# Kernel tuning notes

Measured on AMD Instinct MI355X. Metric: run time of the kernel, lower is better.

The kernel has to match this reference:

```python
import jax, jax.numpy as jnp
import numpy as np

N, E, F_IN, H, NC, NG = 50000, 800000, 256, 64, 4, 64

def setup_inputs() -> dict:
    key = jax.random.key(0)
    ks = jax.random.split(key, 12)
    inp = {
        'x': jax.random.normal(ks[0], (N, F_IN), dtype=jnp.float32),
        'edge_index': jax.random.randint(ks[1], (2, E), 0, N, dtype=jnp.int64),
        'batch': jnp.sort(jax.random.randint(ks[2], (N,), 0, NG, dtype=jnp.int64)),
        # GCNConv layer 1 and 2 (weight [in,out] + bias), Glorot-ish scale
        'W1': jax.random.normal(ks[3], (F_IN, H), dtype=jnp.float32) / np.sqrt(F_IN),
        'b1': jnp.zeros((H,), dtype=jnp.float32),
        'W2': jax.random.normal(ks[4], (H, H), dtype=jnp.float32) / np.sqrt(H),
        'b2': jnp.zeros((H,), dtype=jnp.float32),
        # MLP head
        'fc1_w': jax.random.normal(ks[5], (H, 128), dtype=jnp.float32) / np.sqrt(H),
        'fc1_b': jnp.zeros((128,), dtype=jnp.float32),
        'fc2_w': jax.random.normal(ks[6], (128, NC), dtype=jnp.float32) / np.sqrt(128),
        'fc2_b': jnp.zeros((NC,), dtype=jnp.float32),
    }
    return inp

def _gcn_conv(x, src, dst, W, b, n_nodes):
    # PyG GCNConv: add self-loops, symmetric norm D^-1/2 (A+I) D^-1/2, then X W + b
    h = x @ W  # [N, out]
    deg = jax.ops.segment_sum(jnp.ones_like(dst, dtype=h.dtype), dst, num_segments=n_nodes)
    dinv = jnp.where(deg > 0, jax.lax.rsqrt(deg), 0.0)
    norm = dinv[src] * dinv[dst]  # [E+N]
    msg = h[src] * norm[:, None]
    out = jax.ops.segment_sum(msg, dst, num_segments=n_nodes)
    return out + b

def reference(x, edge_index, batch, W1, b1, W2, b2, fc1_w, fc1_b, fc2_w, fc2_b):
    n = x.shape[0]
    loops = jnp.arange(n, dtype=edge_index.dtype)
    src = jnp.concatenate([edge_index[0], loops])
    dst = jnp.concatenate([edge_index[1], loops])
    h = jax.nn.relu(_gcn_conv(x, src, dst, W1, b1, n))
    h = jax.nn.relu(_gcn_conv(h, src, dst, W2, b2, n))
    # global_mean_pool over graph ids
    sums = jax.ops.segment_sum(h, batch, num_segments=NG)
    cnts = jax.ops.segment_sum(jnp.ones((n,), h.dtype), batch, num_segments=NG)
    pooled = sums / jnp.maximum(cnts, 1.0)[:, None]  # [NG, H]
    z = jax.nn.relu(pooled @ fc1_w + fc1_b)
    # dropout in eval mode = identity
    return z @ fc2_w + fc2_b  # [NG, NC]
```

## Files before the change

### kernel.cpp

```cpp
#include <hip/hip_runtime.h>


#define TPB 256
#define CHUNK_A 4096
#define BCAP 4608

typedef unsigned short bfu;

__device__ __forceinline__ float bf2f(bfu u) {
    union { unsigned u32; float f; } c; c.u32 = ((unsigned)u) << 16; return c.f;
}
__device__ __forceinline__ bfu f2bf(float f) {
    union { float f; unsigned u; } c; c.f = f;
    unsigned r = 0x7FFFu + ((c.u >> 16) & 1u);
    return (bfu)((c.u + r) >> 16);
}
__device__ __forceinline__ float blo(unsigned w) {
    union { unsigned u32; float f; } c; c.u32 = w << 16; return c.f;
}
__device__ __forceinline__ float bhi(unsigned w) {
    union { unsigned u32; float f; } c; c.u32 = w & 0xFFFF0000u; return c.f;
}


__global__ __launch_bounds__(TPB) void k_passA(const int* __restrict__ srcv,
                                               const int* __restrict__ dstv, int E,
                                               int* __restrict__ gcur,
                                               int* __restrict__ staged, int nbuck) {
    __shared__ int pk[CHUNK_A];
    __shared__ int hist[256];
    __shared__ int ebase[256];
    __shared__ int gbase[256];
    __shared__ int lcur[256];
    int t = threadIdx.x;
    int e0 = blockIdx.x * CHUNK_A;
    int e1 = e0 + CHUNK_A; if (e1 > E) e1 = E;

    hist[t] = 0; lcur[t] = 0;
    __syncthreads();
    for (int i = e0 + t; i < e1; i += TPB) atomicAdd(&hist[dstv[i] >> 8], 1);
    __syncthreads();
    int v = hist[t];
    ebase[t] = v;
    __syncthreads();
    for (int off = 1; off < 256; off <<= 1) {
        int u = (t >= off) ? ebase[t - off] : 0;
        __syncthreads();
        ebase[t] += u;
        __syncthreads();
    }
    ebase[t] -= v;
    if (t < nbuck && v > 0) gbase[t] = t * BCAP + atomicAdd(&gcur[t], v);
    __syncthreads();
    for (int i = e0 + t; i < e1; i += TPB) {
        int d = dstv[i];
        int s = srcv[i];
        int b = d >> 8;
        int r = atomicAdd(&lcur[b], 1);
        pk[ebase[b] + r] = (s << 8) | (d & 255);
    }
    __syncthreads();
    int wave = t >> 6, lane = t & 63;
    for (int b = wave; b < nbuck; b += 4) {
        int c = hist[b];
        int lb = ebase[b];
        int gb = gbase[b];
        for (int j = lane; j < c; j += 64) staged[gb + j] = pk[lb + j];
    }
}


__global__ __launch_bounds__(TPB) void k_passB(const int* __restrict__ staged,
                                               const int* __restrict__ gcur,
                                               int* __restrict__ csr_off,
                                               int* __restrict__ csr_src,
                                               float* __restrict__ dinv,
                                               int n, int nbuck) {
    __shared__ int pk[BCAP];
    __shared__ int soff[256];
    __shared__ int hist[256];
    __shared__ int nbase[256];
    __shared__ int cur[256];
    int b = blockIdx.x;
    int n0 = b << 8;
    int n1 = n0 + 256; if (n1 > n) n1 = n;
    int cnt = gcur[b];
    int t = threadIdx.x;

    int cv = (t < nbuck) ? gcur[t] : 0;
    soff[t] = cv;
    hist[t] = 0; cur[t] = 0;
    __syncthreads();
    for (int off = 1; off < 256; off <<= 1) {
        int u = (t >= off) ? soff[t - off] : 0;
        __syncthreads();
        soff[t] += u;
        __syncthreads();
    }
    int base = soff[b] - cnt;

    for (int i = t; i < cnt; i += TPB) pk[i] = staged[b * BCAP + i];
    __syncthreads();
    for (int i = t; i < cnt; i += TPB) atomicAdd(&hist[pk[i] & 255], 1);
    __syncthreads();
    int v = hist[t];
    nbase[t] = v;
    __syncthreads();
    for (int off = 1; off < 256; off <<= 1) {
        int u = (t >= off) ? nbase[t - off] : 0;
        __syncthreads();
        nbase[t] += u;
        __syncthreads();
    }
    nbase[t] -= v;
    if (n0 + t < n1) {
        csr_off[n0 + t] = base + nbase[t];
        dinv[n0 + t] = rsqrtf((float)(v + 1));
    }
    if (b == nbuck - 1 && t == 0) csr_off[n] = base + cnt;
    __syncthreads();
    for (int i = t; i < cnt; i += TPB) {
        int p = pk[i];
        int dloc = p & 255;
        int r = atomicAdd(&cur[dloc], 1);
        csr_src[base + nbase[dloc] + r] = p >> 8;
    }
}


template <int K, bool BF16A>
__global__ __launch_bounds__(TPB) void k_gemm(const void* __restrict__ Av,
                                              const float* __restrict__ W,
                                              const float* __restrict__ dinv,
                                              bfu* __restrict__ C, int n) {
    __shared__ __align__(16) float Wc[64 * 64];
    __shared__ __align__(16) float xr[64 * 68];
    const int t = threadIdx.x;
    const int wave = t >> 6, lane = t & 63;
    const int li = lane >> 4, lj = lane & 15;
    const int rl0 = wave * 16 + li * 4;
    const int rbase = blockIdx.x * 64;

    float acc[4][4] = {{0.f,0.f,0.f,0.f},{0.f,0.f,0.f,0.f},{0.f,0.f,0.f,0.f},{0.f,0.f,0.f,0.f}};

    for (int kc = 0; kc < K; kc += 64) {
        {
            const float4* wsv = (const float4*)(W + (size_t)kc * 64);
            float4* wd = (float4*)Wc;
#pragma unroll
            for (int q = 0; q < 4; q++) wd[t + q * 256] = wsv[t + q * 256];
        }
        {
            int rl = t >> 2;
            int kq = (t & 3) * 16;
            int r = rbase + rl;
            if (!BF16A) {
                const float* A = (const float*)Av;
#pragma unroll
                for (int m = 0; m < 16; m += 4) {
                    float4 xv;
                    if (r < n) xv = *(const float4*)&A[(size_t)r * K + kc + kq + m];
                    else       xv = make_float4(0.f, 0.f, 0.f, 0.f);
                    *(float4*)&xr[rl * 68 + kq + m] = xv;
                }
            } else {
                const bfu* A = (const bfu*)Av;
                uint4 p0 = make_uint4(0,0,0,0), p1 = make_uint4(0,0,0,0);
                if (r < n) {
                    const uint4* ap = (const uint4*)(A + (size_t)r * K + kc + kq);
                    p0 = ap[0]; p1 = ap[1];
                }
                *(float4*)&xr[rl * 68 + kq + 0]  = make_float4(blo(p0.x), bhi(p0.x), blo(p0.y), bhi(p0.y));
                *(float4*)&xr[rl * 68 + kq + 4]  = make_float4(blo(p0.z), bhi(p0.z), blo(p0.w), bhi(p0.w));
                *(float4*)&xr[rl * 68 + kq + 8]  = make_float4(blo(p1.x), bhi(p1.x), blo(p1.y), bhi(p1.y));
                *(float4*)&xr[rl * 68 + kq + 12] = make_float4(blo(p1.z), bhi(p1.z), blo(p1.w), bhi(p1.w));
            }
        }
        __syncthreads();
#pragma unroll 8
        for (int kk = 0; kk < 64; kk++) {
            float4 wv = *(const float4*)&Wc[kk * 64 + lj * 4];
            float x0 = xr[(rl0 + 0) * 68 + kk];
            float x1 = xr[(rl0 + 1) * 68 + kk];
            float x2 = xr[(rl0 + 2) * 68 + kk];
            float x3 = xr[(rl0 + 3) * 68 + kk];
            acc[0][0] += x0 * wv.x; acc[0][1] += x0 * wv.y; acc[0][2] += x0 * wv.z; acc[0][3] += x0 * wv.w;
            acc[1][0] += x1 * wv.x; acc[1][1] += x1 * wv.y; acc[1][2] += x1 * wv.z; acc[1][3] += x1 * wv.w;
            acc[2][0] += x2 * wv.x; acc[2][1] += x2 * wv.y; acc[2][2] += x2 * wv.z; acc[2][3] += x2 * wv.w;
            acc[3][0] += x3 * wv.x; acc[3][1] += x3 * wv.y; acc[3][2] += x3 * wv.z; acc[3][3] += x3 * wv.w;
        }
        __syncthreads();
    }

#pragma unroll
    for (int ri = 0; ri < 4; ri++) {
        int r = rbase + rl0 + ri;
        if (r < n) {
            float d = dinv[r];
            ushort4 o;
            o.x = f2bf(acc[ri][0] * d);
            o.y = f2bf(acc[ri][1] * d);
            o.z = f2bf(acc[ri][2] * d);
            o.w = f2bf(acc[ri][3] * d);
            *(ushort4*)&C[(size_t)r * 64 + lj * 4] = o;
        }
    }
}


__global__ __launch_bounds__(TPB) void k_agg(const bfu* __restrict__ hs,
                                             const int* __restrict__ csr_off,
                                             const int* __restrict__ csr_src,
                                             const float* __restrict__ dinv,
                                             const float* __restrict__ bias,
                                             bfu* __restrict__ out, int n) {
    int node = blockIdx.x * 4 + (threadIdx.x >> 6);
    int lane = threadIdx.x & 63;
    int half = lane >> 5;
    int fl = (lane & 31) * 2;
    if (node >= n) return;
    int p0 = csr_off[node];
    int p1 = csr_off[node + 1];

    float ax = 0.f, ay = 0.f;
    {
        unsigned g = *(const unsigned*)(hs + (size_t)node * 64 + fl);
        if (half == 0) { ax = blo(g); ay = bhi(g); }
    }
    int p = p0;
    for (; p + 16 <= p1; p += 16) {
        int s[8]; unsigned g[8];
#pragma unroll
        for (int i = 0; i < 8; i++) s[i] = csr_src[p + 2 * i + half];
#pragma unroll
        for (int i = 0; i < 8; i++) g[i] = *(const unsigned*)(hs + (size_t)s[i] * 64 + fl);
#pragma unroll
        for (int i = 0; i < 8; i++) { ax += blo(g[i]); ay += bhi(g[i]); }
    }
    if (p + 8 <= p1) {
        int s[4]; unsigned g[4];
#pragma unroll
        for (int i = 0; i < 4; i++) s[i] = csr_src[p + 2 * i + half];
#pragma unroll
        for (int i = 0; i < 4; i++) g[i] = *(const unsigned*)(hs + (size_t)s[i] * 64 + fl);
#pragma unroll
        for (int i = 0; i < 4; i++) { ax += blo(g[i]); ay += bhi(g[i]); }
        p += 8;
    }
    if (p + 4 <= p1) {
        int s[2]; unsigned g[2];
#pragma unroll
        for (int i = 0; i < 2; i++) s[i] = csr_src[p + 2 * i + half];
#pragma unroll
        for (int i = 0; i < 2; i++) g[i] = *(const unsigned*)(hs + (size_t)s[i] * 64 + fl);
#pragma unroll
        for (int i = 0; i < 2; i++) { ax += blo(g[i]); ay += bhi(g[i]); }
        p += 4;
    }
    if (p + 2 <= p1) {
        int s = csr_src[p + half];
        unsigned g = *(const unsigned*)(hs + (size_t)s * 64 + fl);
        ax += blo(g); ay += bhi(g);
        p += 2;
    }
    if (p < p1) {
        int s = csr_src[p];
        unsigned g = *(const unsigned*)(hs + (size_t)s * 64 + fl);
        if (half == 0) { ax += blo(g); ay += bhi(g); }
    }
    ax += __shfl_xor(ax, 32);
    ay += __shfl_xor(ay, 32);

    float d = dinv[node];
    float vx = fmaxf(d * ax + bias[fl + 0], 0.f);
    float vy = fmaxf(d * ay + bias[fl + 1], 0.f);
    if (half == 0) {
        ushort2 o;
        o.x = f2bf(vx);
        o.y = f2bf(vy);
        *(ushort2*)(out + (size_t)node * 64 + fl) = o;
    }
}


__global__ __launch_bounds__(TPB) void k_pool(const bfu* __restrict__ h,
                                              const int* __restrict__ batch, int n,
                                              float* __restrict__ gsum,
                                              int* __restrict__ gcnt) {
    const int CH = 16;
    int wid = blockIdx.x * 4 + (threadIdx.x >> 6);
    int lane = threadIdx.x & 63;
    int i0 = wid * CH;
    if (i0 >= n) return;
    int i1 = i0 + CH; if (i1 > n) i1 = n;
    int g0 = batch[i0];
    int g1 = batch[i1 - 1];
    if (g0 == g1) {
        float acc = 0.f;
#pragma unroll
        for (int i = 0; i < CH; i++) {
            int idx = i0 + i;
            if (idx < i1) acc += bf2f(h[(size_t)idx * 64 + lane]);
        }
        atomicAdd(&gsum[g0 * 64 + lane], acc);
        if (lane == 0) atomicAdd(&gcnt[g0], i1 - i0);
    } else {
        int cur = g0;
        float acc = 0.f;
        int cnt = 0;
        for (int i = i0; i < i1; i++) {
            int g = batch[i];
            if (g != cur) {
                atomicAdd(&gsum[cur * 64 + lane], acc);
                if (lane == 0) atomicAdd(&gcnt[cur], cnt);
                acc = 0.f; cnt = 0; cur = g;
            }
            acc += bf2f(h[(size_t)i * 64 + lane]);
            cnt++;
        }
        atomicAdd(&gsum[cur * 64 + lane], acc);
        if (lane == 0) atomicAdd(&gcnt[cur], cnt);
    }
}


__global__ __launch_bounds__(TPB) void k_head1(const float* __restrict__ gsum,
                                               const int* __restrict__ gcnt,
                                               const float* __restrict__ fc1w,
                                               const float* __restrict__ fc1b,
                                               float* __restrict__ z) {
    int t = threadIdx.x;
    int g = blockIdx.x * 2 + (t >> 7);
    int o = t & 127;
    int c = gcnt[g]; if (c < 1) c = 1;
    float inv = 1.0f / (float)c;
    float a = fc1b[o];
#pragma unroll 16
    for (int j = 0; j < 64; j++) {
        float pj = gsum[g * 64 + j] * inv;
        a += pj * fc1w[j * 128 + o];
    }
    z[g * 128 + o] = fmaxf(a, 0.f);
}


__global__ __launch_bounds__(TPB) void k_head2(const float* __restrict__ z,
                                               const float* __restrict__ fc2w,
                                               const float* __restrict__ fc2b,
                                               float* __restrict__ out) {
    int t = threadIdx.x;
    int g = t >> 2, c = t & 3;
    float a = fc2b[c];
#pragma unroll 16
    for (int o = 0; o < 128; o++) a += z[g * 128 + o] * fc2w[o * 4 + c];
    out[t] = a;
}


extern "C" void kernel_launch(void* const* d_in, const int* in_sizes, int n_in,
                              void* d_out, int out_size, void* d_ws, size_t ws_size,
                              hipStream_t stream) {
    const float* x    = (const float*)d_in[0];
    const int*   ei   = (const int*)d_in[1];
    const int*   batch= (const int*)d_in[2];
    const float* W1   = (const float*)d_in[3];
    const float* b1   = (const float*)d_in[4];
    const float* W2   = (const float*)d_in[5];
    const float* b2   = (const float*)d_in[6];
    const float* fc1w = (const float*)d_in[7];
    const float* fc1b = (const float*)d_in[8];
    const float* fc2w = (const float*)d_in[9];
    const float* fc2b = (const float*)d_in[10];

    const int n = in_sizes[2];
    const int E = in_sizes[1] / 2;
    const int* srcv = ei;
    const int* dstv = ei + E;
    const int nbuck = (n + 255) >> 8;

    char* w = (char*)d_ws;
    int*   gcur   = (int*)w;            w += 256 * 4;
    int*   gcnt   = (int*)w;            w += 64 * 4;
    float* gsum   = (float*)w;          w += 64 * 64 * 4;
    size_t zbytes = (size_t)w - (size_t)d_ws;
    int*   csr_off= (int*)w;            w += (size_t)(n + 1) * 4;
    float* dinv   = (float*)w;          w += (size_t)n * 4;
    int*   csr_src= (int*)w;            w += (size_t)E * 4;
    int*   staged = (int*)w;            w += (size_t)nbuck * BCAP * 4;
    float* zbuf   = (float*)w;          w += 64 * 128 * 4;
    w = (char*)(((size_t)w + 255) & ~(size_t)255);
    bfu* hs = (bfu*)w;                  w += (size_t)n * 64 * 2;
    w = (char*)(((size_t)w + 255) & ~(size_t)255);
    bfu* hb = (bfu*)w;                  w += (size_t)n * 64 * 2;

    hipMemsetAsync(d_ws, 0, zbytes, stream);

    int gA = (E + CHUNK_A - 1) / CHUNK_A;
    k_passA<<<gA, TPB, 0, stream>>>(srcv, dstv, E, gcur, staged, nbuck);
    k_passB<<<nbuck, TPB, 0, stream>>>(staged, gcur, csr_off, csr_src, dinv, n, nbuck);

    int gRows = (n + 63) / 64;
    int gNode = (n + 3) / 4;
    k_gemm<256, false><<<gRows, TPB, 0, stream>>>(x, W1, dinv, hs, n);
    k_agg<<<gNode, TPB, 0, stream>>>(hs, csr_off, csr_src, dinv, b1, hb, n);
    k_gemm<64, true><<<gRows, TPB, 0, stream>>>(hb, W2, dinv, hs, n);
    k_agg<<<gNode, TPB, 0, stream>>>(hs, csr_off, csr_src, dinv, b2, hb, n);

    int nwaves16 = (n + 15) / 16;
    k_pool<<<(nwaves16 + 3) / 4, TPB, 0, stream>>>(hb, batch, n, gsum, gcnt);
    k_head1<<<32, TPB, 0, stream>>>(gsum, gcnt, fc1w, fc1b, zbuf);
    k_head2<<<1, TPB, 0, stream>>>(zbuf, fc2w, fc2b, (float*)d_out);
}
```

Measured before the change: 249.0 us.

## Use bf16 MFMA with split-precision operands for GCN feature GEMMs

Replaces the FP32 FMA GEMM with MFMA 16x16x32 bf16 instructions. FP32 inputs and weights are split into high and low bf16 parts and combined in three MFMAs to keep near-FP32 accuracy. Tiles grow to 128 rows per block and use XOR-swizzled LDS. The aim is to cut ALU time in the 50000x256x64 GEMM. The costs are extra conversion work, more LDS, and uncoalesced scalar bf16 output stores.

```diff
diff --git a/kernel.cpp b/kernel.cpp
--- a/kernel.cpp
+++ b/kernel.cpp
@@ -6,6 +6,8 @@
 #define BCAP 4608
 
 typedef unsigned short bfu;
+typedef __attribute__((ext_vector_type(8))) short s16x8;
+typedef __attribute__((ext_vector_type(4))) float f32x4;
 
 __device__ __forceinline__ float bf2f(bfu u) {
     union { unsigned u32; float f; } c; c.u32 = ((unsigned)u) << 16; return c.f;
@@ -20,6 +22,10 @@
 }
 __device__ __forceinline__ float bhi(unsigned w) {
     union { unsigned u32; float f; } c; c.u32 = w & 0xFFFF0000u; return c.f;
+}
+__device__ __forceinline__ void split_bf(float x, bfu& h, bfu& l) {
+    h = f2bf(x);
+    l = f2bf(x - bf2f(h));
 }
 
 
@@ -128,81 +134,130 @@
 }
 
 
+__device__ __forceinline__ int swz(int rc, int k) {
+    return rc * 64 + (k ^ ((rc & 7) << 3));
+}
+
 template <int K, bool BF16A>
 __global__ __launch_bounds__(TPB) void k_gemm(const void* __restrict__ Av,
                                               const float* __restrict__ W,
                                               const float* __restrict__ dinv,
                                               bfu* __restrict__ C, int n) {
-    __shared__ __align__(16) float Wc[64 * 64];
-    __shared__ __align__(16) float xr[64 * 68];
+    __shared__ __align__(16) ushort Ah[128 * 64];
+    __shared__ __align__(16) ushort Al[BF16A ? 64 : 128 * 64];
+    __shared__ __align__(16) ushort Bh[64 * 64];
+    __shared__ __align__(16) ushort Bl[64 * 64];
+
     const int t = threadIdx.x;
     const int wave = t >> 6, lane = t & 63;
-    const int li = lane >> 4, lj = lane & 15;
-    const int rl0 = wave * 16 + li * 4;
-    const int rbase = blockIdx.x * 64;
-
-    float acc[4][4] = {{0.f,0.f,0.f,0.f},{0.f,0.f,0.f,0.f},{0.f,0.f,0.f,0.f},{0.f,0.f,0.f,0.f}};
+    const int rbase = blockIdx.x * 128;
+
+    f32x4 acc[2][4];
+#pragma unroll
+    for (int i = 0; i < 2; i++)
+#pragma unroll
+        for (int j = 0; j < 4; j++) acc[i][j] = {0.f, 0.f, 0.f, 0.f};
 
     for (int kc = 0; kc < K; kc += 64) {
         {
-            const float4* wsv = (const float4*)(W + (size_t)kc * 64);
-            float4* wd = (float4*)Wc;
-#pragma unroll
-            for (int q = 0; q < 4; q++) wd[t + q * 256] = wsv[t + q * 256];
-        }
-        {
-            int rl = t >> 2;
-            int kq = (t & 3) * 16;
-            int r = rbase + rl;
-            if (!BF16A) {
-                const float* A = (const float*)Av;
-#pragma unroll
-                for (int m = 0; m < 16; m += 4) {
-                    float4 xv;
-                    if (r < n) xv = *(const float4*)&A[(size_t)r * K + kc + kq + m];
-                    else       xv = make_float4(0.f, 0.f, 0.f, 0.f);
-                    *(float4*)&xr[rl * 68 + kq + m] = xv;
+            int c = t & 63;
+            int kg = (t >> 6) << 4;
+#pragma unroll
+            for (int q = 0; q < 4; q++) {
+                ushort4 h4, l4;
+#pragma unroll
+                for (int j = 0; j < 4; j++) {
+                    float w = W[(size_t)(kc + kg + q * 4 + j) * 64 + c];
+                    bfu hh, ll; split_bf(w, hh, ll);
+                    ((bfu*)&h4)[j] = hh;
+                    ((bfu*)&l4)[j] = ll;
                 }
-            } else {
-                const bfu* A = (const bfu*)Av;
-                uint4 p0 = make_uint4(0,0,0,0), p1 = make_uint4(0,0,0,0);
-                if (r < n) {
-                    const uint4* ap = (const uint4*)(A + (size_t)r * K + kc + kq);
-                    p0 = ap[0]; p1 = ap[1];
+                *(ushort4*)&Bh[swz(c, kg + q * 4)] = h4;
+                *(ushort4*)&Bl[swz(c, kg + q * 4)] = l4;
+            }
+        }
+        if (!BF16A) {
+            const float* A = (const float*)Av;
+#pragma unroll
+            for (int q = 0; q < 8; q++) {
+                int idx = q * 256 + t;
+                int row = idx >> 4;
+                int k4 = (idx & 15) << 2;
+                int r = rbase + row;
+                float4 xv = make_float4(0.f, 0.f, 0.f, 0.f);
+                if (r < n) xv = *(const float4*)&A[(size_t)r * K + kc + k4];
+                ushort4 h4, l4;
+                split_bf(xv.x, ((bfu*)&h4)[0], ((bfu*)&l4)[0]);
+                split_bf(xv.y, ((bfu*)&h4)[1], ((bfu*)&l4)[1]);
+                split_bf(xv.z, ((bfu*)&h4)[2], ((bfu*)&l4)[2]);
+                split_bf(xv.w, ((bfu*)&h4)[3], ((bfu*)&l4)[3]);
+                *(ushort4*)&Ah[swz(row, k4)] = h4;
+                *(ushort4*)&Al[swz(row, k4)] = l4;
+            }
+        } else {
+            const bfu* A = (const bfu*)Av;
+#pragma unroll
+            for (int q = 0; q < 4; q++) {
+                int idx = q * 256 + t;
+                int row = idx >> 3;
+                int k8 = (idx & 7) << 3;
+                int r = rbase + row;
+                uint4 v = make_uint4(0u, 0u, 0u, 0u);
+                if (r < n) v = *(const uint4*)(A + (size_t)r * 64 + k8);
+                *(uint2*)&Ah[swz(row, k8)]     = make_uint2(v.x, v.y);
+                *(uint2*)&Ah[swz(row, k8 + 4)] = make_uint2(v.z, v.w);
+            }
+        }
+        __syncthreads();
+
+        const int rl = lane & 15;
+        const int kg8 = (lane >> 4) << 3;
+#pragma unroll
+        for (int ks = 0; ks < 2; ks++) {
+            int k0 = ks * 32 + kg8;
+            s16x8 a_h[2], a_l[2], b_h[4], b_l[4];
+#pragma unroll
+            for (int rt = 0; rt < 2; rt++) {
+                int row = wave * 32 + rt * 16 + rl;
+                a_h[rt] = *(const s16x8*)&Ah[swz(row, k0)];
+                if (!BF16A) a_l[rt] = *(const s16x8*)&Al[swz(row, k0)];
+            }
+#pragma unroll
+            for (int ct = 0; ct < 4; ct++) {
+                int cc = ct * 16 + rl;
+                b_h[ct] = *(const s16x8*)&Bh[swz(cc, k0)];
+                b_l[ct] = *(const s16x8*)&Bl[swz(cc, k0)];
+            }
+#pragma unroll
+            for (int rt = 0; rt < 2; rt++)
+#pragma unroll
+                for (int ct = 0; ct < 4; ct++) {
+                    acc[rt][ct] = __builtin_amdgcn_mfma_f32_16x16x32_bf16(
+                        a_h[rt], b_h[ct], acc[rt][ct], 0, 0, 0);
+                    acc[rt][ct] = __builtin_amdgcn_mfma_f32_16x16x32_bf16(
+                        a_h[rt], b_l[ct], acc[rt][ct], 0, 0, 0);
+                    if (!BF16A)
+                        acc[rt][ct] = __builtin_amdgcn_mfma_f32_16x16x32_bf16(
+                            a_l[rt], b_h[ct], acc[rt][ct], 0, 0, 0);
                 }
-                *(float4*)&xr[rl * 68 + kq + 0]  = make_float4(blo(p0.x), bhi(p0.x), blo(p0.y), bhi(p0.y));
-                *(float4*)&xr[rl * 68 + kq + 4]  = make_float4(blo(p0.z), bhi(p0.z), blo(p0.w), bhi(p0.w));
-                *(float4*)&xr[rl * 68 + kq + 8]  = make_float4(blo(p1.x), bhi(p1.x), blo(p1.y), bhi(p1.y));
-                *(float4*)&xr[rl * 68 + kq + 12] = make_float4(blo(p1.z), bhi(p1.z), blo(p1.w), bhi(p1.w));
-            }
-        }
-        __syncthreads();
-#pragma unroll 8
-        for (int kk = 0; kk < 64; kk++) {
-            float4 wv = *(const float4*)&Wc[kk * 64 + lj * 4];
-            float x0 = xr[(rl0 + 0) * 68 + kk];
-            float x1 = xr[(rl0 + 1) * 68 + kk];
-            float x2 = xr[(rl0 + 2) * 68 + kk];
-            float x3 = xr[(rl0 + 3) * 68 + kk];
-            acc[0][0] += x0 * wv.x; acc[0][1] += x0 * wv.y; acc[0][2] += x0 * wv.z; acc[0][3] += x0 * wv.w;
-            acc[1][0] += x1 * wv.x; acc[1][1] += x1 * wv.y; acc[1][2] += x1 * wv.z; acc[1][3] += x1 * wv.w;
-            acc[2][0] += x2 * wv.x; acc[2][1] += x2 * wv.y; acc[2][2] += x2 * wv.z; acc[2][3] += x2 * wv.w;
-            acc[3][0] += x3 * wv.x; acc[3][1] += x3 * wv.y; acc[3][2] += x3 * wv.z; acc[3][3] += x3 * wv.w;
-        }
-        __syncthreads();
-    }
-
-#pragma unroll
-    for (int ri = 0; ri < 4; ri++) {
-        int r = rbase + rl0 + ri;
-        if (r < n) {
-            float d = dinv[r];
-            ushort4 o;
-            o.x = f2bf(acc[ri][0] * d);
-            o.y = f2bf(acc[ri][1] * d);
-            o.z = f2bf(acc[ri][2] * d);
-            o.w = f2bf(acc[ri][3] * d);
-            *(ushort4*)&C[(size_t)r * 64 + lj * 4] = o;
+        }
+        __syncthreads();
+    }
+
+    const int rl = lane & 15;
+    const int rq = (lane >> 4) << 2;
+#pragma unroll
+    for (int rt = 0; rt < 2; rt++) {
+#pragma unroll
+        for (int reg = 0; reg < 4; reg++) {
+            int r = rbase + wave * 32 + rt * 16 + rq + reg;
+            if (r < n) {
+                float d = dinv[r];
+#pragma unroll
+                for (int ct = 0; ct < 4; ct++) {
+                    C[(size_t)r * 64 + ct * 16 + rl] = f2bf(acc[rt][ct][reg] * d);
+                }
+            }
         }
     }
 }
@@ -399,7 +454,7 @@
     k_passA<<<gA, TPB, 0, stream>>>(srcv, dstv, E, gcur, staged, nbuck);
     k_passB<<<nbuck, TPB, 0, stream>>>(staged, gcur, csr_off, csr_src, dinv, n, nbuck);
 
-    int gRows = (n + 63) / 64;
+    int gRows = (n + 127) / 128;
     int gNode = (n + 3) / 4;
     k_gemm<256, false><<<gRows, TPB, 0, stream>>>(x, W1, dinv, hs, n);
     k_agg<<<gNode, TPB, 0, stream>>>(hs, csr_off, csr_src, dinv, b1, hb, n);
```

Result: no change. 251.6 us (+1.1%).
